# Performance work log

Hardware: AMD Instinct MI355X
Metric: run time of the kernel (lower is better)

Reference implementation:

```python
import jax, jax.numpy as jnp
import numpy as np

N_NODES = 100000
N_EDGES = 1600000
IN_CH = 500
H1, C1 = 8, 8           # layer 1: 8 heads x 8 dims, concat -> 64
H2, C2 = 8, 3           # layer 2: 8 heads x 3 classes, mean over heads
NEG_SLOPE = 0.2         # PyG GATConv default


def gat_layer(x, src, dst, W, a_src, a_dst, b, concat):
    """PyG-style GATConv (self-loops already included in src/dst)."""
    N = x.shape[0]
    H, C = a_src.shape
    xw = (x @ W).reshape(N, H, C)                      # [N,H,C]
    al_src = jnp.einsum('nhc,hc->nh', xw, a_src)       # [N,H]
    al_dst = jnp.einsum('nhc,hc->nh', xw, a_dst)       # [N,H]
    e = jax.nn.leaky_relu(al_src[src] + al_dst[dst], NEG_SLOPE)  # [E,H]
    # segment softmax over incoming edges of each destination node
    m = jax.lax.stop_gradient(jax.ops.segment_max(e, dst, num_segments=N))
    ex = jnp.exp(e - m[dst])
    s = jax.ops.segment_sum(ex, dst, num_segments=N)
    alpha = ex / (s[dst] + 1e-16)                      # [E,H]
    out = jax.ops.segment_sum(alpha[:, :, None] * xw[src], dst, num_segments=N)  # [N,H,C]
    out = out.reshape(N, H * C) if concat else out.mean(axis=1)
    return out + b


def setup_inputs() -> dict:
    key = jax.random.key(0)
    ks = jax.random.split(key, 10)
    x = jax.random.normal(ks[0], (N_NODES, IN_CH), dtype=jnp.float32)
    edge_index = jax.random.randint(ks[1], (2, N_EDGES), 0, N_NODES, dtype=jnp.int64)
    sc1 = 1.0 / np.sqrt(IN_CH)
    sc2 = 1.0 / np.sqrt(H1 * C1)
    W1 = jax.random.normal(ks[2], (IN_CH, H1 * C1), dtype=jnp.float32) * sc1
    a1_src = jax.random.normal(ks[3], (H1, C1), dtype=jnp.float32) * 0.1
    a1_dst = jax.random.normal(ks[4], (H1, C1), dtype=jnp.float32) * 0.1
    b1 = jnp.zeros((H1 * C1,), dtype=jnp.float32)
    W2 = jax.random.normal(ks[5], (H1 * C1, H2 * C2), dtype=jnp.float32) * sc2
    a2_src = jax.random.normal(ks[6], (H2, C2), dtype=jnp.float32) * 0.1
    a2_dst = jax.random.normal(ks[7], (H2, C2), dtype=jnp.float32) * 0.1
    b2 = jnp.zeros((C2,), dtype=jnp.float32)
    return {"x": x, "W1": W1, "a1_src": a1_src, "a1_dst": a1_dst, "b1": b1,
            "W2": W2, "a2_src": a2_src, "a2_dst": a2_dst, "b2": b2,
            "edge_index": edge_index}


def reference(x, W1, a1_src, a1_dst, b1, W2, a2_src, a2_dst, b2, edge_index):
    N = x.shape[0]
    loop = jnp.arange(N, dtype=edge_index.dtype)   # PyG add_self_loops=True
    src = jnp.concatenate([edge_index[0], loop])
    dst = jnp.concatenate([edge_index[1], loop])
    h = jax.nn.elu(gat_layer(x, src, dst, W1, a1_src, a1_dst, b1, concat=True))
    out = gat_layer(h, src, dst, W2, a2_src, a2_dst, b2, concat=False)
    return jax.nn.softmax(out, axis=1)
```

## Files before the change

### kernel.cpp

```cpp
#include <hip/hip_runtime.h>
#include <math.h>

#define N_NODESC 100000
#define N_EDGESC 1600000
#define E_TOT    1700000
#define IN_CH    500
#define KPAD     512
#define D1 64
#define D2 24
#define D2P 32
#define NBKT 391
#define CAP  5120
#define EPB  4096
#define NPB  416
#define WPB  32

typedef __attribute__((ext_vector_type(8))) short short8;
typedef __attribute__((ext_vector_type(4))) float f32x4;

__device__ inline short f2bf(float f) {
    unsigned u = __float_as_uint(f);
    u += 0x7fffu + ((u >> 16) & 1u);
    return (short)(u >> 16);
}
__device__ inline unsigned pkbf(float a, float b) {
    const unsigned ua = __float_as_uint(a) + 0x8000u;
    const unsigned ub = __float_as_uint(b) + 0x8000u;
    return __builtin_amdgcn_perm(ub, ua, 0x07060302u);
}
__device__ inline float bflo(unsigned u) { return __uint_as_float(u << 16); }
__device__ inline float bfhi(unsigned u) { return __uint_as_float(u & 0xffff0000u); }

__global__ __launch_bounds__(256) void k_part2(const int* __restrict__ ei,
                                               int* __restrict__ gcnt,
                                               int* __restrict__ tmp,
                                               const float* __restrict__ W1,
                                               short* __restrict__ wT) {
    const int t = threadIdx.x;
    if (blockIdx.x >= NPB) {
        const int wb = blockIdx.x - NPB;
#pragma unroll
        for (int r = 0; r < 4; r++) {
            const int idx = wb * 1024 + r * 256 + t;
            const int n = idx >> 9, k = idx & (KPAD - 1);
            wT[idx] = (k < IN_CH) ? f2bf(W1[k * D1 + n]) : (short)0;
        }
        return;
    }
    __shared__ int hist[NBKT];
    __shared__ int lbase[NBKT];
    const int e0 = blockIdx.x * EPB;
    for (int i = t; i < NBKT; i += 256) hist[i] = 0;
    __syncthreads();
    int se[16], de[16], mo[16];
#pragma unroll
    for (int i = 0; i < 16; i++) {
        const int e = e0 + i * 256 + t;
        int s = -1, d = 0;
        if (e < E_TOT) {
            if (e < N_EDGESC) { s = ei[e]; d = ei[N_EDGESC + e]; }
            else { s = d = e - N_EDGESC; }
        }
        se[i] = s; de[i] = d;
        mo[i] = (s >= 0) ? atomicAdd(&hist[d >> 8], 1) : 0;
    }
    __syncthreads();
    for (int i = t; i < NBKT; i += 256)
        lbase[i] = hist[i] ? (i * CAP + atomicAdd(&gcnt[i * 32], hist[i])) : 0;
    __syncthreads();
#pragma unroll
    for (int i = 0; i < 16; i++) {
        if (se[i] >= 0) {
            const int b = de[i] >> 8;
            const int idx = lbase[b] + mo[i];
            if (idx < (b + 1) * CAP)
                tmp[idx] = se[i] | ((de[i] & 255) << 17);
        }
    }
}

__global__ __launch_bounds__(256) void k_bucket2(const int* __restrict__ gcnt,
                                                 const int* __restrict__ tmp,
                                                 int* __restrict__ off,
                                                 int* __restrict__ srt) {
    __shared__ int se[CAP];
    __shared__ int cnts[256];
    __shared__ int sc[256];
    __shared__ int lcur[256];
    __shared__ int red[4];
    __shared__ int sbase;
    const int b = blockIdx.x;
    const int t = threadIdx.x;
    const int cnt = min(gcnt[b * 32], CAP);

    int pre = 0;
    if (t < b) pre += min(gcnt[t * 32], CAP);
    if (t + 256 < b) pre += min(gcnt[(t + 256) * 32], CAP);
#pragma unroll
    for (int m = 1; m < 64; m <<= 1) pre += __shfl_xor(pre, m, 64);
    if ((t & 63) == 0) red[t >> 6] = pre;
    cnts[t] = 0;
    __syncthreads();
    if (t == 0) sbase = red[0] + red[1] + red[2] + red[3];
    __syncthreads();
    const int base = sbase;

    for (int i = t; i < cnt; i += 256) {
        const int p = tmp[b * CAP + i];
        se[i] = p;
        atomicAdd(&cnts[p >> 17], 1);
    }
    __syncthreads();
    sc[t] = cnts[t];
    __syncthreads();
    for (int d = 1; d < 256; d <<= 1) {
        const int u = (t >= d) ? sc[t - d] : 0;
        __syncthreads();
        sc[t] += u;
        __syncthreads();
    }
    const int excl = base + sc[t] - cnts[t];
    const int nodeBase = b << 8;
    const int nNodes = min(256, N_NODESC - nodeBase);
    if (t < nNodes) off[nodeBase + t] = excl;
    lcur[t] = excl;
    if (b == 0 && t == 0) off[N_NODESC] = E_TOT;
    __syncthreads();
    for (int i = t; i < cnt; i += 256) {
        const int p = se[i];
        const int pos = atomicAdd(&lcur[p >> 17], 1);
        srt[pos] = p & 0x1FFFF;
    }
}

__global__ __launch_bounds__(256) void k_gemm1(const float* __restrict__ x,
                                               const short* __restrict__ wT,
                                               const float* __restrict__ a1s,
                                               const float* __restrict__ a1d,
                                               short* __restrict__ xw1b,
                                               float* __restrict__ al1s,
                                               float* __restrict__ al1d) {
    __shared__ short xs[32 * 520];
    const int t = threadIdx.x;
    const int rowBase = blockIdx.x * 32;
    const int r = t >> 3, j = t & 7;
    const float* xr = x + (long)(rowBase + r) * IN_CH;
    short* xrow = xs + r * 520;
#pragma unroll
    for (int i = 0; i < 16; i++) {
        const int c = j + i * 8;
        if (c < 125) {
            const float4 v = *(const float4*)(xr + c * 4);
            const unsigned lo = pkbf(v.x, v.y);
            const unsigned hi = pkbf(v.z, v.w);
            *(uint2*)(xrow + c * 4) = make_uint2(lo, hi);
        }
    }
    if (j < 6) *(unsigned*)(xrow + 500 + j * 2) = 0u;
    __syncthreads();

    const int lane = t & 63, wv = t >> 6;
    const int m = lane & 15, kg = lane >> 4;
    f32x4 acc[2];
    acc[0] = (f32x4){0.f, 0.f, 0.f, 0.f};
    acc[1] = (f32x4){0.f, 0.f, 0.f, 0.f};
    const short* wcol = wT + (wv * 16 + m) * KPAD;
#pragma unroll
    for (int k0 = 0; k0 < KPAD; k0 += 32) {
        const short8 bf = *(const short8*)(wcol + k0 + kg * 8);
#pragma unroll
        for (int mf = 0; mf < 2; mf++) {
            const short8 af = *(const short8*)(xs + (mf * 16 + m) * 520 + k0 + kg * 8);
            acc[mf] = __builtin_amdgcn_mfma_f32_16x16x32_bf16(af, bf, acc[mf], 0, 0, 0);
        }
    }
    const int col = wv * 16 + m;
    const float as = a1s[col];
    const float ad = a1d[col];
    const int hh = wv * 2 + (m >> 3);
#pragma unroll
    for (int mf = 0; mf < 2; mf++) {
#pragma unroll
        for (int jj = 0; jj < 4; jj++) {
            const int row = rowBase + mf * 16 + kg * 4 + jj;
            const float v = acc[mf][jj];
            xw1b[(long)row * D1 + col] = f2bf(v);
            float ts = v * as, td = v * ad;
            ts += __shfl_xor(ts, 1, 64); td += __shfl_xor(td, 1, 64);
            ts += __shfl_xor(ts, 2, 64); td += __shfl_xor(td, 2, 64);
            ts += __shfl_xor(ts, 4, 64); td += __shfl_xor(td, 4, 64);
            if ((m & 7) == 0) {
                al1s[row * 8 + hh] = ts;
                al1d[row * 8 + hh] = td;
            }
        }
    }
}

__global__ __launch_bounds__(256) void k_gat1(const int* __restrict__ off,
                                              const int* __restrict__ srt_src,
                                              const float* __restrict__ al1s,
                                              const float* __restrict__ al1d,
                                              const short* __restrict__ xw1b,
                                              const float* __restrict__ b1,
                                              const float* __restrict__ W2,
                                              const float* __restrict__ a2s,
                                              const float* __restrict__ a2d,
                                              float* __restrict__ xw2,
                                              float* __restrict__ al2s,
                                              float* __restrict__ al2d) {
    __shared__ float w2s[D1 * D2];
    __shared__ float hrow[4][D1];
    const int tid = threadIdx.x;
    for (int i = tid; i < D1 * D2; i += 256) w2s[i] = W2[i];
    __syncthreads();

    const int lane = tid & 63;
    const int wid = tid >> 6;
    const int n = blockIdx.x * 4 + wid;
    const int esub = lane >> 4;
    const int q = lane & 15;
    const int h = q >> 1;

    const float ald = al1d[n * 8 + h];
    const int kend = off[n + 1];

    float4 acc = make_float4(0.f, 0.f, 0.f, 0.f);
    float ssum = 0.f;
    int k = off[n] + esub;
    int s = (k < kend) ? srt_src[k] : -1;
    while (s >= 0) {
        const int kn = k + 4;
        const int sn = (kn < kend) ? srt_src[kn] : -1;
        float ev = al1s[s * 8 + h] + ald;
        ev = ev > 0.f ? ev : 0.2f * ev;
        const float ex = __expf(ev);
        const uint2 v = *(const uint2*)(xw1b + (long)s * D1 + q * 4);
        acc.x += ex * bflo(v.x); acc.y += ex * bfhi(v.x);
        acc.z += ex * bflo(v.y); acc.w += ex * bfhi(v.y);
        ssum += ex;
        k = kn; s = sn;
    }
#pragma unroll
    for (int mm = 16; mm < 64; mm <<= 1) {
        acc.x += __shfl_xor(acc.x, mm, 64);
        acc.y += __shfl_xor(acc.y, mm, 64);
        acc.z += __shfl_xor(acc.z, mm, 64);
        acc.w += __shfl_xor(acc.w, mm, 64);
        ssum  += __shfl_xor(ssum,  mm, 64);
    }
    if (esub == 0) {
        const float inv = 1.0f / (ssum + 1e-16f);
        const float4 bb = *(const float4*)(b1 + q * 4);
        float4 rr;
        rr.x = acc.x * inv + bb.x; rr.x = rr.x > 0.f ? rr.x : expm1f(rr.x);
        rr.y = acc.y * inv + bb.y; rr.y = rr.y > 0.f ? rr.y : expm1f(rr.y);
        rr.z = acc.z * inv + bb.z; rr.z = rr.z > 0.f ? rr.z : expm1f(rr.z);
        rr.w = acc.w * inv + bb.w; rr.w = rr.w > 0.f ? rr.w : expm1f(rr.w);
        *(float4*)(&hrow[wid][q * 4]) = rr;
    }
    const int half = lane / 24;
    const int j2 = lane - half * 24;
    const int cb = (half == 1) ? 32 : 0;
    float o = 0.f;
#pragma unroll
    for (int c4 = 0; c4 < 8; c4++) {
        const float4 hv = *(const float4*)(&hrow[wid][cb + c4 * 4]);
        const float* wr = w2s + (cb + c4 * 4) * D2 + j2;
        o += hv.x * wr[0] + hv.y * wr[D2] + hv.z * wr[2 * D2] + hv.w * wr[3 * D2];
    }
    const int src2 = (lane < 24) ? lane + 24 : lane;
    o += __shfl(o, src2, 64);
    if (lane < 24) xw2[(long)n * D2P + lane] = o;
    const float ps = o * a2s[j2];
    const float pd = o * a2d[j2];
    const int hb = 3 * (lane & 7);
    const float s3 = __shfl(ps, hb, 64) + __shfl(ps, hb + 1, 64) + __shfl(ps, hb + 2, 64);
    const float d3 = __shfl(pd, hb, 64) + __shfl(pd, hb + 1, 64) + __shfl(pd, hb + 2, 64);
    if (lane < 8) {
        al2s[n * 8 + lane] = s3;
        al2d[n * 8 + lane] = d3;
    }
}

__global__ __launch_bounds__(256) void k_gat2(const int* __restrict__ off,
                                              const int* __restrict__ srt_src,
                                              const float* __restrict__ al2s,
                                              const float* __restrict__ al2d,
                                              const float* __restrict__ xw2,
                                              const float* __restrict__ b2,
                                              float* __restrict__ out) {
    __shared__ float sm[4][24];
    const int tid = threadIdx.x;
    const int lane = tid & 63;
    const int wid = tid >> 6;
    const int n = blockIdx.x * 4 + wid;
    const int esub = lane / 24;
    const int j = lane - esub * 24;
    const int h = j / 3;

    float acc = 0.f, ssum = 0.f;
    if (esub < 2) {
        const float ald = al2d[n * 8 + h];
        const int kend = off[n + 1];
        int k = off[n] + esub;
        int s = (k < kend) ? srt_src[k] : -1;
        while (s >= 0) {
            const int kn = k + 2;
            const int sn = (kn < kend) ? srt_src[kn] : -1;
            float ev = al2s[s * 8 + h] + ald;
            ev = ev > 0.f ? ev : 0.2f * ev;
            const float ex = __expf(ev);
            acc += ex * xw2[(long)s * D2P + j];
            ssum += ex;
            k = kn; s = sn;
        }
    }
    acc  += __shfl_down(acc, 24, 64);
    ssum += __shfl_down(ssum, 24, 64);
    if (lane < 24) sm[wid][j] = acc / (ssum + 1e-16f);
    __syncthreads();
    float lg = 0.f;
    if (lane < 3) {
#pragma unroll
        for (int hh = 0; hh < 8; hh++) lg += sm[wid][hh * 3 + lane];
        lg = lg * 0.125f + b2[lane];
    }
    const float l0 = __shfl(lg, 0, 64);
    const float l1 = __shfl(lg, 1, 64);
    const float l2 = __shfl(lg, 2, 64);
    if (lane < 3) {
        const float m = fmaxf(l0, fmaxf(l1, l2));
        const float denom = expf(l0 - m) + expf(l1 - m) + expf(l2 - m);
        out[(long)n * 3 + lane] = expf(lg - m) / denom;
    }
}

extern "C" void kernel_launch(void* const* d_in, const int* in_sizes, int n_in,
                              void* d_out, int out_size, void* d_ws, size_t ws_size,
                              hipStream_t stream) {
    const float* x   = (const float*)d_in[0];
    const float* W1  = (const float*)d_in[1];
    const float* a1s = (const float*)d_in[2];
    const float* a1d = (const float*)d_in[3];
    const float* b1  = (const float*)d_in[4];
    const float* W2  = (const float*)d_in[5];
    const float* a2s = (const float*)d_in[6];
    const float* a2d = (const float*)d_in[7];
    const float* b2  = (const float*)d_in[8];
    const int*   ei  = (const int*)d_in[9];
    float* out = (float*)d_out;

    float* ws   = (float*)d_ws;
    float* xw2  = ws;
    float* al1s = xw2  + 3200000;
    float* al1d = al1s + 800000;
    float* al2s = al1d + 800000;
    float* al2d = al2s + 800000;
    short* xw1b = (short*)(al2d + 800000);
    int* off    = (int*)(xw1b + 6400000);
    int* gcnt   = off + 100004;
    int* srt    = gcnt + NBKT * 32;
    short* wT   = (short*)(srt + 1700000);
    int* tmp    = (int*)xw2;

    hipMemsetAsync(gcnt, 0, (size_t)NBKT * 32 * sizeof(int), stream);

    k_part2<<<NPB + WPB, 256, 0, stream>>>(ei, gcnt, tmp, W1, wT);
    k_bucket2<<<NBKT, 256, 0, stream>>>(gcnt, tmp, off, srt);
    k_gemm1<<<N_NODESC / 32, 256, 0, stream>>>(x, wT, a1s, a1d, xw1b, al1s, al1d);
    k_gat1<<<N_NODESC / 4, 256, 0, stream>>>(off, srt, al1s, al1d, xw1b, b1,
                                             W2, a2s, a2d, xw2, al2s, al2d);
    k_gat2<<<N_NODESC / 4, 256, 0, stream>>>(off, srt, al2s, al2d, xw2, b2, out);
}
```

Measured before the change: 515.0 us.

## Remap aggregation lanes to one head per lane with 8 edges in flight

Both GAT aggregation kernels now assign lane&7 to a head and lane>>3 to an edge slot, so each wavefront processes 8 edges per iteration instead of 4 (layer 1) or 2 (layer 2). Each lane does one al1s/al2s lookup and one exp per edge, then reads a wider vector load of that head's features (16B bf16 in layer 1, a float4 in layer 2). The layer-2 xw2 buffer is relaid out so each head's 3 values are padded to 4, which allows the float4 loads. Layer 2 drops its shared memory and __syncthreads in favour of shuffle reductions. The aim is more memory-level parallelism and fewer redundant exps, at the cost of more shuffles and more registers.

```diff
diff --git a/kernel.cpp b/kernel.cpp
--- a/kernel.cpp
+++ b/kernel.cpp
@@ -218,46 +218,54 @@
     const int lane = tid & 63;
     const int wid = tid >> 6;
     const int n = blockIdx.x * 4 + wid;
-    const int esub = lane >> 4;
-    const int q = lane & 15;
-    const int h = q >> 1;
-
-    const float ald = al1d[n * 8 + h];
+    const int e8 = lane >> 3;
+    const int hd = lane & 7;
+
+    const float ald = al1d[n * 8 + hd];
     const int kend = off[n + 1];
 
-    float4 acc = make_float4(0.f, 0.f, 0.f, 0.f);
+    float4 a0 = make_float4(0.f, 0.f, 0.f, 0.f);
+    float4 a1 = make_float4(0.f, 0.f, 0.f, 0.f);
     float ssum = 0.f;
-    int k = off[n] + esub;
+    int k = off[n] + e8;
     int s = (k < kend) ? srt_src[k] : -1;
     while (s >= 0) {
-        const int kn = k + 4;
+        const int kn = k + 8;
         const int sn = (kn < kend) ? srt_src[kn] : -1;
-        float ev = al1s[s * 8 + h] + ald;
+        float ev = al1s[s * 8 + hd] + ald;
         ev = ev > 0.f ? ev : 0.2f * ev;
         const float ex = __expf(ev);
-        const uint2 v = *(const uint2*)(xw1b + (long)s * D1 + q * 4);
-        acc.x += ex * bflo(v.x); acc.y += ex * bfhi(v.x);
-        acc.z += ex * bflo(v.y); acc.w += ex * bfhi(v.y);
+        const uint4 v = *(const uint4*)(xw1b + (long)s * D1 + hd * 8);
+        a0.x += ex * bflo(v.x); a0.y += ex * bfhi(v.x);
+        a0.z += ex * bflo(v.y); a0.w += ex * bfhi(v.y);
+        a1.x += ex * bflo(v.z); a1.y += ex * bfhi(v.z);
+        a1.z += ex * bflo(v.w); a1.w += ex * bfhi(v.w);
         ssum += ex;
         k = kn; s = sn;
     }
 #pragma unroll
-    for (int mm = 16; mm < 64; mm <<= 1) {
-        acc.x += __shfl_xor(acc.x, mm, 64);
-        acc.y += __shfl_xor(acc.y, mm, 64);
-        acc.z += __shfl_xor(acc.z, mm, 64);
-        acc.w += __shfl_xor(acc.w, mm, 64);
+    for (int mm = 8; mm < 64; mm <<= 1) {
+        a0.x += __shfl_xor(a0.x, mm, 64); a0.y += __shfl_xor(a0.y, mm, 64);
+        a0.z += __shfl_xor(a0.z, mm, 64); a0.w += __shfl_xor(a0.w, mm, 64);
+        a1.x += __shfl_xor(a1.x, mm, 64); a1.y += __shfl_xor(a1.y, mm, 64);
+        a1.z += __shfl_xor(a1.z, mm, 64); a1.w += __shfl_xor(a1.w, mm, 64);
         ssum  += __shfl_xor(ssum,  mm, 64);
     }
-    if (esub == 0) {
-        const float inv = 1.0f / (ssum + 1e-16f);
-        const float4 bb = *(const float4*)(b1 + q * 4);
-        float4 rr;
-        rr.x = acc.x * inv + bb.x; rr.x = rr.x > 0.f ? rr.x : expm1f(rr.x);
-        rr.y = acc.y * inv + bb.y; rr.y = rr.y > 0.f ? rr.y : expm1f(rr.y);
-        rr.z = acc.z * inv + bb.z; rr.z = rr.z > 0.f ? rr.z : expm1f(rr.z);
-        rr.w = acc.w * inv + bb.w; rr.w = rr.w > 0.f ? rr.w : expm1f(rr.w);
-        *(float4*)(&hrow[wid][q * 4]) = rr;
+    const float inv = 1.0f / (ssum + 1e-16f);
+    const float4 bb0 = *(const float4*)(b1 + hd * 8);
+    const float4 bb1 = *(const float4*)(b1 + hd * 8 + 4);
+    float4 r0, r1;
+    r0.x = a0.x * inv + bb0.x; r0.x = r0.x > 0.f ? r0.x : expm1f(r0.x);
+    r0.y = a0.y * inv + bb0.y; r0.y = r0.y > 0.f ? r0.y : expm1f(r0.y);
+    r0.z = a0.z * inv + bb0.z; r0.z = r0.z > 0.f ? r0.z : expm1f(r0.z);
+    r0.w = a0.w * inv + bb0.w; r0.w = r0.w > 0.f ? r0.w : expm1f(r0.w);
+    r1.x = a1.x * inv + bb1.x; r1.x = r1.x > 0.f ? r1.x : expm1f(r1.x);
+    r1.y = a1.y * inv + bb1.y; r1.y = r1.y > 0.f ? r1.y : expm1f(r1.y);
+    r1.z = a1.z * inv + bb1.z; r1.z = r1.z > 0.f ? r1.z : expm1f(r1.z);
+    r1.w = a1.w * inv + bb1.w; r1.w = r1.w > 0.f ? r1.w : expm1f(r1.w);
+    if (e8 == 0) {
+        *(float4*)(&hrow[wid][hd * 8])     = r0;
+        *(float4*)(&hrow[wid][hd * 8 + 4]) = r1;
     }
     const int half = lane / 24;
     const int j2 = lane - half * 24;
@@ -271,7 +279,10 @@
     }
     const int src2 = (lane < 24) ? lane + 24 : lane;
     o += __shfl(o, src2, 64);
-    if (lane < 24) xw2[(long)n * D2P + lane] = o;
+    if (lane < 24) {
+        const int h3 = j2 / 3;
+        xw2[(long)n * D2P + h3 * 4 + (j2 - 3 * h3)] = o;
+    }
     const float ps = o * a2s[j2];
     const float pd = o * a2d[j2];
     const int hb = 3 * (lane & 7);
@@ -290,49 +301,54 @@
                                               const float* __restrict__ xw2,
                                               const float* __restrict__ b2,
                                               float* __restrict__ out) {
-    __shared__ float sm[4][24];
     const int tid = threadIdx.x;
     const int lane = tid & 63;
     const int wid = tid >> 6;
     const int n = blockIdx.x * 4 + wid;
-    const int esub = lane / 24;
-    const int j = lane - esub * 24;
-    const int h = j / 3;
-
-    float acc = 0.f, ssum = 0.f;
-    if (esub < 2) {
-        const float ald = al2d[n * 8 + h];
-        const int kend = off[n + 1];
-        int k = off[n] + esub;
-        int s = (k < kend) ? srt_src[k] : -1;
-        while (s >= 0) {
-            const int kn = k + 2;
-            const int sn = (kn < kend) ? srt_src[kn] : -1;
-            float ev = al2s[s * 8 + h] + ald;
-            ev = ev > 0.f ? ev : 0.2f * ev;
-            const float ex = __expf(ev);
-            acc += ex * xw2[(long)s * D2P + j];
-            ssum += ex;
-            k = kn; s = sn;
-        }
-    }
-    acc  += __shfl_down(acc, 24, 64);
-    ssum += __shfl_down(ssum, 24, 64);
-    if (lane < 24) sm[wid][j] = acc / (ssum + 1e-16f);
-    __syncthreads();
-    float lg = 0.f;
+    const int e8 = lane >> 3;
+    const int hd = lane & 7;
+
+    const float ald = al2d[n * 8 + hd];
+    const int kend = off[n + 1];
+
+    float ax = 0.f, ay = 0.f, az = 0.f, ssum = 0.f;
+    int k = off[n] + e8;
+    int s = (k < kend) ? srt_src[k] : -1;
+    while (s >= 0) {
+        const int kn = k + 8;
+        const int sn = (kn < kend) ? srt_src[kn] : -1;
+        float ev = al2s[s * 8 + hd] + ald;
+        ev = ev > 0.f ? ev : 0.2f * ev;
+        const float ex = __expf(ev);
+        const float4 v = *(const float4*)(xw2 + (long)s * D2P + hd * 4);
+        ax += ex * v.x; ay += ex * v.y; az += ex * v.z;
+        ssum += ex;
+        k = kn; s = sn;
+    }
+#pragma unroll
+    for (int mm = 8; mm < 64; mm <<= 1) {
+        ax += __shfl_xor(ax, mm, 64);
+        ay += __shfl_xor(ay, mm, 64);
+        az += __shfl_xor(az, mm, 64);
+        ssum += __shfl_xor(ssum, mm, 64);
+    }
+    const float inv = 1.0f / (ssum + 1e-16f);
+    float mx = ax * inv, my = ay * inv, mz = az * inv;
+#pragma unroll
+    for (int mm = 1; mm < 8; mm <<= 1) {
+        mx += __shfl_xor(mx, mm, 64);
+        my += __shfl_xor(my, mm, 64);
+        mz += __shfl_xor(mz, mm, 64);
+    }
+    const float l0 = mx * 0.125f + b2[0];
+    const float l1 = my * 0.125f + b2[1];
+    const float l2 = mz * 0.125f + b2[2];
+    const float mmax = fmaxf(l0, fmaxf(l1, l2));
+    const float ee0 = expf(l0 - mmax), ee1 = expf(l1 - mmax), ee2 = expf(l2 - mmax);
+    const float dinv = 1.0f / (ee0 + ee1 + ee2);
     if (lane < 3) {
-#pragma unroll
-        for (int hh = 0; hh < 8; hh++) lg += sm[wid][hh * 3 + lane];
-        lg = lg * 0.125f + b2[lane];
-    }
-    const float l0 = __shfl(lg, 0, 64);
-    const float l1 = __shfl(lg, 1, 64);
-    const float l2 = __shfl(lg, 2, 64);
-    if (lane < 3) {
-        const float m = fmaxf(l0, fmaxf(l1, l2));
-        const float denom = expf(l0 - m) + expf(l1 - m) + expf(l2 - m);
-        out[(long)n * 3 + lane] = expf(lg - m) / denom;
+        const float p = (lane == 0) ? ee0 : (lane == 1) ? ee1 : ee2;
+        out[(long)n * 3 + lane] = p * dinv;
     }
 }
 
```

Result: faster. 483.4 us (-6.1%).
